# Kernel optimization log

Hardware: AMD Instinct MI355X
Metric: run time of the kernel (lower is better)

The kernel has to match this reference:

```python
import jax, jax.numpy as jnp
import numpy as np

H, W, C = 56, 56, 384
WS, SHIFT, HEADS = 7, 3, 12
HEAD_DIM = C // HEADS
SCALE = HEAD_DIM ** (-0.5)
NWIN = (H // WS) * (W // WS)  # 64 windows per image
NTOK = WS * WS                # 49 tokens per window
EPS = 1e-5


def _gen_mask():
    # static shift-window attention mask, computed with numpy (jit-safe constant)
    img = np.zeros((H, W))
    sl = (slice(0, -WS), slice(-WS, -SHIFT), slice(-SHIFT, None))
    cnt = 0
    for hs in sl:
        for ws in sl:
            img[hs, ws] = cnt
            cnt += 1
    mw = img.reshape(H // WS, WS, W // WS, WS).transpose(0, 2, 1, 3).reshape(-1, NTOK)
    diff = mw[:, None, :] - mw[:, :, None]  # (NWIN, NTOK, NTOK)
    return jnp.asarray(np.where(diff != 0, -100.0, 0.0), dtype=jnp.float32)

ATTN_MASK = _gen_mask()


def _layernorm(x, g, b):
    mu = jnp.mean(x, axis=-1, keepdims=True)
    var = jnp.var(x, axis=-1, keepdims=True)
    return (x - mu) * jax.lax.rsqrt(var + EPS) * g + b


def setup_inputs() -> dict:
    key = jax.random.key(0)
    ks = jax.random.split(key, 6)
    s = 0.02
    return {
        "x": jax.random.normal(ks[0], (16, H * W, C), dtype=jnp.float32),
        "ln1_g": jnp.ones((C,), jnp.float32),
        "ln1_b": jnp.zeros((C,), jnp.float32),
        "qkv_w": jax.random.normal(ks[1], (C, 3 * C), jnp.float32) * s,
        "proj_w": jax.random.normal(ks[2], (C, C), jnp.float32) * s,
        "proj_b": jnp.zeros((C,), jnp.float32),
        "ln2_g": jnp.ones((C,), jnp.float32),
        "ln2_b": jnp.zeros((C,), jnp.float32),
        "fc1_w": jax.random.normal(ks[3], (C, 4 * C), jnp.float32) * s,
        "fc1_b": jnp.zeros((4 * C,), jnp.float32),
        "fc2_w": jax.random.normal(ks[4], (4 * C, C), jnp.float32) * s,
        "fc2_b": jnp.zeros((C,), jnp.float32),
    }


def reference(x, ln1_g, ln1_b, qkv_w, proj_w, proj_b, ln2_g, ln2_b, fc1_w, fc1_b, fc2_w, fc2_b):
    B, N, _ = x.shape
    h = x
    y = _layernorm(x, ln1_g, ln1_b).reshape(B, H, W, C)
    # cyclic shift (note: source never rolls back; we match it)
    y = jnp.roll(y, shift=(-SHIFT, -SHIFT), axis=(1, 2))
    # window partition -> (B*NWIN, NTOK, C)
    y = y.reshape(B, H // WS, WS, W // WS, WS, C).transpose(0, 1, 3, 2, 4, 5)
    y = y.reshape(B * NWIN, NTOK, C)
    # qkv (no bias), split heads
    qkv = (y @ qkv_w).reshape(B * NWIN, NTOK, 3, HEADS, HEAD_DIM)
    qkv = qkv.transpose(2, 0, 3, 1, 4)  # (3, BW, heads, NTOK, hd)
    q, k, v = qkv[0], qkv[1], qkv[2]
    attn = jnp.einsum('whnd,whmd->whnm', q, k) * SCALE  # (BW, heads, NTOK, NTOK)
    attn = attn.reshape(B, NWIN, HEADS, NTOK, NTOK) + ATTN_MASK[None, :, None]
    attn = jax.nn.softmax(attn.reshape(B * NWIN, HEADS, NTOK, NTOK), axis=-1)
    o = jnp.einsum('whnm,whmd->whnd', attn, v)
    o = o.transpose(0, 2, 1, 3).reshape(B * NWIN, NTOK, C)
    o = o @ proj_w + proj_b
    # window reverse -> (B, N, C)
    o = o.reshape(B, H // WS, W // WS, WS, WS, C).transpose(0, 1, 3, 2, 4, 5)
    o = o.reshape(B, N, C)
    x1 = h + o
    # MLP (GELU after both fc1 and fc2, as in source)
    m = _layernorm(x1, ln2_g, ln2_b)
    m = jax.nn.gelu(m @ fc1_w + fc1_b, approximate=False)
    m = jax.nn.gelu(m @ fc2_w + fc2_b, approximate=False)
    return x1 + m
```

## Files before the change

kernel.cpp:

```cpp
#include <hip/hip_runtime.h>
#include <hip/hip_bf16.h>
#include <cstdint>
#include <cstddef>

#define C_DIM   384
#define NIMG    3136
#define MROWS   50176
#define QK_SCALE 0.17677669529663687f

using bf16x8 = __attribute__((ext_vector_type(8))) short;
using f32x4  = __attribute__((ext_vector_type(4))) float;

__device__ __forceinline__ short f2bf(float f) {
  union { float f; uint32_t u; } v; v.f = f;
  uint32_t r = (v.u + 0x7fffu + ((v.u >> 16) & 1u)) >> 16;
  return (short)(uint16_t)r;
}

__device__ __forceinline__ float bf2f(short s) {
  union { uint32_t u; float f; } v; v.u = ((uint32_t)(uint16_t)s) << 16;
  return v.f;
}

__device__ __forceinline__ void async_copy16(const void* g, void* l) {
  __builtin_amdgcn_global_load_lds(
      (const __attribute__((address_space(1))) void*)g,
      (__attribute__((address_space(3))) void*)l, 16, 0, 0);
}

__device__ __forceinline__ float gelu_fast(float x) {
  float x2 = x * x;
  float u = fmaf(0.0356774081f, x2, 0.7978845608f);
  float e = exp2f(x * u * 2.8853900818f);
  float r = __builtin_amdgcn_rcpf(e + 1.0f);
  return fmaf(-x, r, x);
}

__global__ __launch_bounds__(256) void transpose_cast(
    const float* __restrict__ w, short* __restrict__ wt, int K, int N) {
  int idx = blockIdx.x * 256 + threadIdx.x;
  if (idx >= K * N) return;
  int k = idx / N;
  int n = idx - k * N;
  wt[(size_t)n * K + k] = f2bf(w[idx]);
}

template <typename IN>
__global__ __launch_bounds__(256) void ln_kernel(
    const IN* __restrict__ x, const float* __restrict__ g,
    const float* __restrict__ b, short* __restrict__ y, int windowed) {
  int token = blockIdx.x * 4 + (threadIdx.x >> 6);
  int lane = threadIdx.x & 63;
  size_t src;
  if (windowed) {
    int bw = token / 49;
    int tt = token - bw * 49;
    int bb = bw >> 6, w = bw & 63;
    int hs = (w >> 3) * 7 + tt / 7 + 3; if (hs >= 56) hs -= 56;
    int ws = (w & 7) * 7 + (tt % 7) + 3; if (ws >= 56) ws -= 56;
    src = (size_t)(bb * NIMG + hs * 56 + ws) * C_DIM;
  } else {
    src = (size_t)token * C_DIM;
  }
  const IN* xr = x + src;
  float v[6];
  float s = 0.f;
#pragma unroll
  for (int i = 0; i < 6; ++i) {
    if constexpr (sizeof(IN) == 4) v[i] = (float)xr[lane + i * 64];
    else v[i] = bf2f((short)xr[lane + i * 64]);
    s += v[i];
  }
#pragma unroll
  for (int m = 1; m < 64; m <<= 1) s += __shfl_xor(s, m);
  float mu = s * (1.0f / 384.0f);
  float var = 0.f;
#pragma unroll
  for (int i = 0; i < 6; ++i) { float d = v[i] - mu; var += d * d; }
#pragma unroll
  for (int m = 1; m < 64; m <<= 1) var += __shfl_xor(var, m);
  float rstd = rsqrtf(var * (1.0f / 384.0f) + 1e-5f);
  short* yr = y + (size_t)token * C_DIM;
#pragma unroll
  for (int i = 0; i < 6; ++i) {
    int c = lane + i * 64;
    yr[c] = f2bf((v[i] - mu) * rstd * g[c] + b[c]);
  }
}

template <int EPI>
__device__ __forceinline__ void gemm_epilogue(
    f32x4 (&acc)[4][4], void* Out, const float* bias, const void* resid,
    int N, int m0, int n0, int wm, int wn, int lrow, int quad) {
#pragma unroll
  for (int i = 0; i < 4; ++i) {
#pragma unroll
    for (int r = 0; r < 4; ++r) {
      int row = m0 + wm * 64 + i * 16 + quad * 4 + r;
      if (EPI == 1) {
        int bw = row / 49;
        int tt = row - bw * 49;
        int bb = bw >> 6, w = bw & 63;
        int nimg = ((w >> 3) * 7 + tt / 7) * 56 + (w & 7) * 7 + (tt % 7);
        size_t obase = ((size_t)(bb * NIMG + nimg)) * C_DIM;
#pragma unroll
        for (int j = 0; j < 4; ++j) {
          int col = n0 + wn * 64 + j * 16 + lrow;
          size_t oi = obase + col;
          ((short*)Out)[oi] =
              f2bf(acc[i][j][r] + bias[col] + ((const float*)resid)[oi]);
        }
      } else {
#pragma unroll
        for (int j = 0; j < 4; ++j) {
          int col = n0 + wn * 64 + j * 16 + lrow;
          float v = acc[i][j][r];
          if (EPI == 0) {
            ((short*)Out)[(size_t)row * N + col] = f2bf(v);
          } else if (EPI == 2) {
            ((short*)Out)[(size_t)row * N + col] = f2bf(gelu_fast(v + bias[col]));
          } else {
            size_t oi = (size_t)row * C_DIM + col;
            ((float*)Out)[oi] =
                bf2f(((const short*)resid)[oi]) + gelu_fast(v + bias[col]);
          }
        }
      }
    }
  }
}

__device__ __forceinline__ void grid_decode(int nby, int& m0, int& n0) {
  const int wg = (int)blockIdx.x;
  const int swz = (wg & 7) * ((int)gridDim.x >> 3) + (wg >> 3);
  const int mb = swz / nby;
  const int nb = swz - mb * nby;
  m0 = mb * 128;
  n0 = nb * 128;
}

template <int EPI>
__global__ __launch_bounds__(256, 4) void gemm_pipe32_kernel(
    const short* __restrict__ A, const short* __restrict__ Bt,
    void* __restrict__ Out, const float* __restrict__ bias,
    const void* __restrict__ resid, int M, int N, int K, int nby) {
  __shared__ __align__(16) short lds[2][128 * 32 * 2];
  const int t = threadIdx.x;
  const int wave = t >> 6, lane = t & 63;
  const int lrow = lane & 15, quad = lane >> 4;
  const int wm = wave & 1, wn = wave >> 1;
  int m0, n0;
  grid_decode(nby, m0, n0);

  f32x4 acc[4][4] = {};
  const int srow = t >> 2;
  const int spos = t & 3;
  const int nt = K >> 5;

  auto stage = [&](int buf, int k0) {
    short* la = &lds[buf][0];
    short* lb = la + 128 * 32;
#pragma unroll
    for (int i = 0; i < 2; ++i) {
      int row = i * 64 + srow;
      int ca = spos ^ ((row >> 1) & 3);
      async_copy16(A + (size_t)(m0 + row) * K + k0 + ca * 8,
                   la + (i * 64 + wave * 16) * 32);
      async_copy16(Bt + (size_t)(n0 + row) * K + k0 + ca * 8,
                   lb + (i * 64 + wave * 16) * 32);
    }
  };

  auto compute = [&](int buf) {
    short* ldsA = &lds[buf][0];
    short* ldsB = ldsA + 128 * 32;
    bf16x8 af[4], bfr[4];
#pragma unroll
    for (int i = 0; i < 4; ++i) {
      int ra = wm * 64 + i * 16 + lrow;
      af[i] = *(const bf16x8*)(ldsA + ra * 32 + ((quad ^ ((ra >> 1) & 3)) * 8));
      int rb = wn * 64 + i * 16 + lrow;
      bfr[i] = *(const bf16x8*)(ldsB + rb * 32 + ((quad ^ ((rb >> 1) & 3)) * 8));
    }
    __builtin_amdgcn_s_setprio(1);
#pragma unroll
    for (int i = 0; i < 4; ++i)
#pragma unroll
      for (int j = 0; j < 4; ++j)
        acc[i][j] = __builtin_amdgcn_mfma_f32_16x16x32_bf16(af[i], bfr[j],
                                                            acc[i][j], 0, 0, 0);
    __builtin_amdgcn_s_setprio(0);
  };

  stage(0, 0);
  for (int kt = 0; kt < nt; ++kt) {
    __builtin_amdgcn_sched_barrier(0);
    if (kt + 1 < nt) {
      stage((kt + 1) & 1, (kt + 1) * 32);
      asm volatile("s_waitcnt vmcnt(4)" ::: "memory");
    } else {
      asm volatile("s_waitcnt vmcnt(0)" ::: "memory");
    }
    __builtin_amdgcn_s_barrier();
    __builtin_amdgcn_sched_barrier(0);
    compute(kt & 1);
    __builtin_amdgcn_sched_barrier(0);
    __builtin_amdgcn_s_barrier();
  }
  gemm_epilogue<EPI>(acc, Out, bias, resid, N, m0, n0, wm, wn, lrow, quad);
}

template <int EPI>
__global__ __launch_bounds__(256, 2) void gemm_pipe64_kernel(
    const short* __restrict__ A, const short* __restrict__ Bt,
    void* __restrict__ Out, const float* __restrict__ bias,
    const void* __restrict__ resid, int M, int N, int K, int nby) {
  __shared__ __align__(16) short lds[2][128 * 64 * 2];
  const int t = threadIdx.x;
  const int wave = t >> 6, lane = t & 63;
  const int lrow = lane & 15, quad = lane >> 4;
  const int wm = wave & 1, wn = wave >> 1;
  int m0, n0;
  grid_decode(nby, m0, n0);

  f32x4 acc[4][4] = {};
  const int srow = t >> 3;
  const int spos = t & 7;
  const int nt = K >> 6;

  auto stage = [&](int buf, int k0) {
    short* la = &lds[buf][0];
    short* lb = la + 128 * 64;
#pragma unroll
    for (int i = 0; i < 4; ++i) {
      int row = i * 32 + srow;
      int ca = spos ^ (row & 7);
      async_copy16(A + (size_t)(m0 + row) * K + k0 + ca * 8,
                   la + (i * 32 + wave * 8) * 64);
      async_copy16(Bt + (size_t)(n0 + row) * K + k0 + ca * 8,
                   lb + (i * 32 + wave * 8) * 64);
    }
  };

  auto compute = [&](int buf) {
    short* ldsA = &lds[buf][0];
    short* ldsB = ldsA + 128 * 64;
#pragma unroll
    for (int ks = 0; ks < 2; ++ks) {
      const int cb = ks * 4;
      bf16x8 af[4], bfr[4];
#pragma unroll
      for (int i = 0; i < 4; ++i) {
        int ra = wm * 64 + i * 16 + lrow;
        af[i] = *(const bf16x8*)(ldsA + ra * 64 + (((cb + quad) ^ (ra & 7)) * 8));
        int rb = wn * 64 + i * 16 + lrow;
        bfr[i] = *(const bf16x8*)(ldsB + rb * 64 + (((cb + quad) ^ (rb & 7)) * 8));
      }
      __builtin_amdgcn_s_setprio(1);
#pragma unroll
      for (int i = 0; i < 4; ++i)
#pragma unroll
        for (int j = 0; j < 4; ++j)
          acc[i][j] = __builtin_amdgcn_mfma_f32_16x16x32_bf16(af[i], bfr[j],
                                                              acc[i][j], 0, 0, 0);
      __builtin_amdgcn_s_setprio(0);
    }
  };

  stage(0, 0);
  for (int kt = 0; kt < nt; ++kt) {
    __builtin_amdgcn_sched_barrier(0);
    if (kt + 1 < nt) {
      stage((kt + 1) & 1, (kt + 1) * 64);
      asm volatile("s_waitcnt vmcnt(8)" ::: "memory");
    } else {
      asm volatile("s_waitcnt vmcnt(0)" ::: "memory");
    }
    __builtin_amdgcn_s_barrier();
    __builtin_amdgcn_sched_barrier(0);
    compute(kt & 1);
    __builtin_amdgcn_sched_barrier(0);
    __builtin_amdgcn_s_barrier();
  }
  gemm_epilogue<EPI>(acc, Out, bias, resid, N, m0, n0, wm, wn, lrow, quad);
}

__global__ __launch_bounds__(256) void attn_kernel(
    const short* __restrict__ qkv, short* __restrict__ o) {
  __shared__ __align__(16) short plds[4][64 * 40];
  __shared__ __align__(16) short vlds[4][32 * 72];
  const int wavei = threadIdx.x >> 6;
  const int lane = threadIdx.x & 63;
  const int gw = blockIdx.x * 4 + wavei;
  const int bw = gw / 12;
  const int h = gw - bw * 12;
  const int w = bw & 63;
  const int lrow = lane & 15, quad = lane >> 4;
  const short* base = qkv + (size_t)bw * 49 * 1152 + h * 32;

  bf16x8 qf[4], kf[4];
#pragma unroll
  for (int i = 0; i < 4; ++i) {
    int tq = i * 16 + lrow;
    const short* p = base + (size_t)tq * 1152 + quad * 8;
    qf[i] = *(const bf16x8*)p;
    kf[i] = *(const bf16x8*)(p + 384);
  }

  short* vw = vlds[wavei];
  {
    bf16x8 vrow[4] = {};
    if (lane < 49) {
      const short* vp = base + 768 + (size_t)lane * 1152;
#pragma unroll
      for (int c = 0; c < 4; ++c) vrow[c] = *(const bf16x8*)(vp + c * 8);
    }
#pragma unroll
    for (int c = 0; c < 4; ++c)
#pragma unroll
      for (int jj = 0; jj < 8; ++jj)
        vw[(c * 8 + jj) * 72 + lane] = vrow[c][jj];
  }

  f32x4 sa[4][4] = {};
#pragma unroll
  for (int i = 0; i < 4; ++i)
#pragma unroll
    for (int j = 0; j < 4; ++j)
      sa[i][j] = __builtin_amdgcn_mfma_f32_16x16x32_bf16(qf[i], kf[j], sa[i][j], 0, 0, 0);

  int tl = lane < 49 ? lane : 0;
  int rr = tl / 7, cc = tl - rr * 7;
  int hs = (w >> 3) * 7 + rr;
  int ws = (w & 7) * 7 + cc;
  int id = (hs < 49 ? 0 : (hs < 53 ? 3 : 6)) + (ws < 49 ? 0 : (ws < 53 ? 1 : 2));

  int idn[4], idm[4][4];
#pragma unroll
  for (int j = 0; j < 4; ++j) idn[j] = __shfl(id, j * 16 + lrow);
#pragma unroll
  for (int i = 0; i < 4; ++i)
#pragma unroll
    for (int r = 0; r < 4; ++r) idm[i][r] = __shfl(id, i * 16 + quad * 4 + r);

#pragma unroll
  for (int i = 0; i < 4; ++i)
#pragma unroll
    for (int j = 0; j < 4; ++j)
#pragma unroll
      for (int r = 0; r < 4; ++r) {
        float v = sa[i][j][r] * QK_SCALE + (idm[i][r] == idn[j] ? 0.f : -100.f);
        sa[i][j][r] = (j * 16 + lrow < 49) ? v : -1e30f;
      }

#pragma unroll
  for (int i = 0; i < 4; ++i)
#pragma unroll
    for (int r = 0; r < 4; ++r) {
      float mx = -1e30f;
#pragma unroll
      for (int j = 0; j < 4; ++j) mx = fmaxf(mx, sa[i][j][r]);
#pragma unroll
      for (int m = 1; m < 16; m <<= 1) mx = fmaxf(mx, __shfl_xor(mx, m));
      float sum = 0.f;
#pragma unroll
      for (int j = 0; j < 4; ++j) {
        float e = exp2f((sa[i][j][r] - mx) * 1.44269504f);
        sa[i][j][r] = e;
        sum += e;
      }
#pragma unroll
      for (int m = 1; m < 16; m <<= 1) sum += __shfl_xor(sum, m);
      float inv = 1.0f / sum;
#pragma unroll
      for (int j = 0; j < 4; ++j) sa[i][j][r] *= inv;
    }

  short* pw = plds[wavei];
  f32x4 oa[4][2] = {};
#pragma unroll
  for (int kk = 0; kk < 2; ++kk) {
#pragma unroll
    for (int jh = 0; jh < 2; ++jh) {
      int j = kk * 2 + jh;
#pragma unroll
      for (int i = 0; i < 4; ++i)
#pragma unroll
        for (int r = 0; r < 4; ++r)
          pw[(i * 16 + quad * 4 + r) * 40 + jh * 16 + lrow] = f2bf(sa[i][j][r]);
    }
    asm volatile("s_waitcnt lgkmcnt(0)" ::: "memory");
    __builtin_amdgcn_sched_barrier(0);

    bf16x8 vf[2];
#pragma unroll
    for (int j2 = 0; j2 < 2; ++j2)
      vf[j2] = *(const bf16x8*)(vw + (j2 * 16 + lrow) * 72 + kk * 32 + quad * 8);
#pragma unroll
    for (int i = 0; i < 4; ++i) {
      bf16x8 pf = *(const bf16x8*)(pw + (i * 16 + lrow) * 40 + quad * 8);
#pragma unroll
      for (int j2 = 0; j2 < 2; ++j2)
        oa[i][j2] = __builtin_amdgcn_mfma_f32_16x16x32_bf16(pf, vf[j2], oa[i][j2], 0, 0, 0);
    }
    asm volatile("s_waitcnt lgkmcnt(0)" ::: "memory");
    __builtin_amdgcn_sched_barrier(0);
  }

#pragma unroll
  for (int i = 0; i < 4; ++i)
#pragma unroll
    for (int j2 = 0; j2 < 2; ++j2)
#pragma unroll
      for (int r = 0; r < 4; ++r) {
        int m = i * 16 + quad * 4 + r;
        if (m < 49)
          o[((size_t)bw * 49 + m) * 384 + h * 32 + j2 * 16 + lrow] = f2bf(oa[i][j2][r]);
      }
}

extern "C" void kernel_launch(void* const* d_in, const int* in_sizes, int n_in,
                              void* d_out, int out_size, void* d_ws, size_t ws_size,
                              hipStream_t stream) {
  const float* x      = (const float*)d_in[0];
  const float* ln1_g  = (const float*)d_in[1];
  const float* ln1_b  = (const float*)d_in[2];
  const float* qkv_w  = (const float*)d_in[3];
  const float* proj_w = (const float*)d_in[4];
  const float* proj_b = (const float*)d_in[5];
  const float* ln2_g  = (const float*)d_in[6];
  const float* ln2_b  = (const float*)d_in[7];
  const float* fc1_w  = (const float*)d_in[8];
  const float* fc1_b  = (const float*)d_in[9];
  const float* fc2_w  = (const float*)d_in[10];
  const float* fc2_b  = (const float*)d_in[11];
  float* out = (float*)d_out;

  char* ws = (char*)d_ws;
  auto alloc = [&](size_t bytes) {
    char* p = ws;
    ws += (bytes + 255) & ~(size_t)255;
    return p;
  };
  short* qkv_wT  = (short*)alloc((size_t)1152 * 384 * 2);
  short* proj_wT = (short*)alloc((size_t)384 * 384 * 2);
  short* fc1_wT  = (short*)alloc((size_t)1536 * 384 * 2);
  short* fc2_wT  = (short*)alloc((size_t)384 * 1536 * 2);
  short* bufA    = (short*)alloc((size_t)MROWS * 384 * 2);
  short* x1      = (short*)alloc((size_t)MROWS * 384 * 2);
  short* bufB    = (short*)alloc((size_t)MROWS * 1536 * 2);

  transpose_cast<<<(384 * 1152) / 256, 256, 0, stream>>>(qkv_w, qkv_wT, 384, 1152);
  transpose_cast<<<(384 * 384) / 256, 256, 0, stream>>>(proj_w, proj_wT, 384, 384);
  transpose_cast<<<(384 * 1536) / 256, 256, 0, stream>>>(fc1_w, fc1_wT, 384, 1536);
  transpose_cast<<<(1536 * 384) / 256, 256, 0, stream>>>(fc2_w, fc2_wT, 1536, 384);

  ln_kernel<float><<<MROWS / 4, 256, 0, stream>>>(x, ln1_g, ln1_b, bufA, 1);

  gemm_pipe32_kernel<0><<<392 * 9, 256, 0, stream>>>(bufA, qkv_wT, bufB, nullptr,
                                                     nullptr, MROWS, 1152, 384, 9);

  attn_kernel<<<3072, 256, 0, stream>>>(bufB, bufA);

  gemm_pipe32_kernel<1><<<392 * 3, 256, 0, stream>>>(bufA, proj_wT, x1, proj_b,
                                                     x, MROWS, 384, 384, 3);

  ln_kernel<short><<<MROWS / 4, 256, 0, stream>>>(x1, ln2_g, ln2_b, bufA, 0);

  gemm_pipe32_kernel<2><<<392 * 12, 256, 0, stream>>>(bufA, fc1_wT, bufB, fc1_b,
                                                      nullptr, MROWS, 1536, 384, 12);

  gemm_pipe64_kernel<3><<<392 * 3, 256, 0, stream>>>(bufB, fc2_wT, out, fc2_b,
                                                     x1, MROWS, 384, 1536, 3);
}
```

Baseline: 521.6 us.

## Load GEMM B operand directly from global into registers, bypassing LDS

```diff
diff --git a/kernel.cpp b/kernel.cpp
--- a/kernel.cpp
+++ b/kernel.cpp
@@ -144,7 +144,7 @@
     const short* __restrict__ A, const short* __restrict__ Bt,
     void* __restrict__ Out, const float* __restrict__ bias,
     const void* __restrict__ resid, int M, int N, int K, int nby) {
-  __shared__ __align__(16) short lds[2][128 * 32 * 2];
+  __shared__ __align__(16) short lds[2][128 * 32];
   const int t = threadIdx.x;
   const int wave = t >> 6, lane = t & 63;
   const int lrow = lane & 15, quad = lane >> 4;
@@ -157,30 +157,32 @@
   const int spos = t & 3;
   const int nt = K >> 5;
 
-  auto stage = [&](int buf, int k0) {
+  auto stageA = [&](int buf, int k0) {
     short* la = &lds[buf][0];
-    short* lb = la + 128 * 32;
 #pragma unroll
     for (int i = 0; i < 2; ++i) {
       int row = i * 64 + srow;
       int ca = spos ^ ((row >> 1) & 3);
       async_copy16(A + (size_t)(m0 + row) * K + k0 + ca * 8,
                    la + (i * 64 + wave * 16) * 32);
-      async_copy16(Bt + (size_t)(n0 + row) * K + k0 + ca * 8,
-                   lb + (i * 64 + wave * 16) * 32);
-    }
-  };
-
-  auto compute = [&](int buf) {
+    }
+  };
+
+  auto loadB = [&](bf16x8 (&b)[4], int k0) {
+#pragma unroll
+    for (int j = 0; j < 4; ++j) {
+      int rb = n0 + wn * 64 + j * 16 + lrow;
+      b[j] = *(const bf16x8*)(Bt + (size_t)rb * K + k0 + quad * 8);
+    }
+  };
+
+  auto compute = [&](int buf, bf16x8 (&bfr)[4]) {
     short* ldsA = &lds[buf][0];
-    short* ldsB = ldsA + 128 * 32;
-    bf16x8 af[4], bfr[4];
+    bf16x8 af[4];
 #pragma unroll
     for (int i = 0; i < 4; ++i) {
       int ra = wm * 64 + i * 16 + lrow;
       af[i] = *(const bf16x8*)(ldsA + ra * 32 + ((quad ^ ((ra >> 1) & 3)) * 8));
-      int rb = wn * 64 + i * 16 + lrow;
-      bfr[i] = *(const bf16x8*)(ldsB + rb * 32 + ((quad ^ ((rb >> 1) & 3)) * 8));
     }
     __builtin_amdgcn_s_setprio(1);
 #pragma unroll
@@ -192,18 +194,30 @@
     __builtin_amdgcn_s_setprio(0);
   };
 
-  stage(0, 0);
-  for (int kt = 0; kt < nt; ++kt) {
-    __builtin_amdgcn_sched_barrier(0);
-    if (kt + 1 < nt) {
-      stage((kt + 1) & 1, (kt + 1) * 32);
-      asm volatile("s_waitcnt vmcnt(4)" ::: "memory");
+  bf16x8 b0[4], b1[4];
+  stageA(0, 0);
+  loadB(b0, 0);
+  for (int kt = 0; kt < nt; kt += 2) {
+    __builtin_amdgcn_sched_barrier(0);
+    stageA(1, (kt + 1) * 32);
+    loadB(b1, (kt + 1) * 32);
+    asm volatile("s_waitcnt vmcnt(6)" ::: "memory");
+    __builtin_amdgcn_s_barrier();
+    __builtin_amdgcn_sched_barrier(0);
+    compute(0, b0);
+    __builtin_amdgcn_sched_barrier(0);
+    __builtin_amdgcn_s_barrier();
+    __builtin_amdgcn_sched_barrier(0);
+    if (kt + 2 < nt) {
+      stageA(0, (kt + 2) * 32);
+      loadB(b0, (kt + 2) * 32);
+      asm volatile("s_waitcnt vmcnt(6)" ::: "memory");
     } else {
       asm volatile("s_waitcnt vmcnt(0)" ::: "memory");
     }
     __builtin_amdgcn_s_barrier();
     __builtin_amdgcn_sched_barrier(0);
-    compute(kt & 1);
+    compute(1, b1);
     __builtin_amdgcn_sched_barrier(0);
     __builtin_amdgcn_s_barrier();
   }
@@ -215,7 +229,7 @@
     const short* __restrict__ A, const short* __restrict__ Bt,
     void* __restrict__ Out, const float* __restrict__ bias,
     const void* __restrict__ resid, int M, int N, int K, int nby) {
-  __shared__ __align__(16) short lds[2][128 * 64 * 2];
+  __shared__ __align__(16) short lds[2][128 * 64];
   const int t = threadIdx.x;
   const int wave = t >> 6, lane = t & 63;
   const int lrow = lane & 15, quad = lane >> 4;
@@ -228,57 +242,74 @@
   const int spos = t & 7;
   const int nt = K >> 6;
 
-  auto stage = [&](int buf, int k0) {
+  auto stageA = [&](int buf, int k0) {
     short* la = &lds[buf][0];
-    short* lb = la + 128 * 64;
 #pragma unroll
     for (int i = 0; i < 4; ++i) {
       int row = i * 32 + srow;
       int ca = spos ^ (row & 7);
       async_copy16(A + (size_t)(m0 + row) * K + k0 + ca * 8,
                    la + (i * 32 + wave * 8) * 64);
-      async_copy16(Bt + (size_t)(n0 + row) * K + k0 + ca * 8,
-                   lb + (i * 32 + wave * 8) * 64);
-    }
-  };
-
-  auto compute = [&](int buf) {
+    }
+  };
+
+  auto loadB = [&](bf16x8 (&b)[2][4], int k0) {
+#pragma unroll
+    for (int ks = 0; ks < 2; ++ks)
+#pragma unroll
+      for (int j = 0; j < 4; ++j) {
+        int rb = n0 + wn * 64 + j * 16 + lrow;
+        b[ks][j] = *(const bf16x8*)(Bt + (size_t)rb * K + k0 + (ks * 4 + quad) * 8);
+      }
+  };
+
+  auto compute = [&](int buf, bf16x8 (&b)[2][4]) {
     short* ldsA = &lds[buf][0];
-    short* ldsB = ldsA + 128 * 64;
 #pragma unroll
     for (int ks = 0; ks < 2; ++ks) {
       const int cb = ks * 4;
-      bf16x8 af[4], bfr[4];
+      bf16x8 af[4];
 #pragma unroll
       for (int i = 0; i < 4; ++i) {
         int ra = wm * 64 + i * 16 + lrow;
         af[i] = *(const bf16x8*)(ldsA + ra * 64 + (((cb + quad) ^ (ra & 7)) * 8));
-        int rb = wn * 64 + i * 16 + lrow;
-        bfr[i] = *(const bf16x8*)(ldsB + rb * 64 + (((cb + quad) ^ (rb & 7)) * 8));
       }
       __builtin_amdgcn_s_setprio(1);
 #pragma unroll
       for (int i = 0; i < 4; ++i)
 #pragma unroll
         for (int j = 0; j < 4; ++j)
-          acc[i][j] = __builtin_amdgcn_mfma_f32_16x16x32_bf16(af[i], bfr[j],
+          acc[i][j] = __builtin_amdgcn_mfma_f32_16x16x32_bf16(af[i], b[ks][j],
                                                               acc[i][j], 0, 0, 0);
       __builtin_amdgcn_s_setprio(0);
     }
   };
 
-  stage(0, 0);
-  for (int kt = 0; kt < nt; ++kt) {
-    __builtin_amdgcn_sched_barrier(0);
-    if (kt + 1 < nt) {
-      stage((kt + 1) & 1, (kt + 1) * 64);
-      asm volatile("s_waitcnt vmcnt(8)" ::: "memory");
+  bf16x8 b0[2][4], b1[2][4];
+  stageA(0, 0);
+  loadB(b0, 0);
+  for (int kt = 0; kt < nt; kt += 2) {
+    __builtin_amdgcn_sched_barrier(0);
+    stageA(1, (kt + 1) * 64);
+    loadB(b1, (kt + 1) * 64);
+    asm volatile("s_waitcnt vmcnt(12)" ::: "memory");
+    __builtin_amdgcn_s_barrier();
+    __builtin_amdgcn_sched_barrier(0);
+    compute(0, b0);
+    __builtin_amdgcn_sched_barrier(0);
+    __builtin_amdgcn_s_barrier();
+
+    __builtin_amdgcn_sched_barrier(0);
+    if (kt + 2 < nt) {
+      stageA(0, (kt + 2) * 64);
+      loadB(b0, (kt + 2) * 64);
+      asm volatile("s_waitcnt vmcnt(12)" ::: "memory");
     } else {
       asm volatile("s_waitcnt vmcnt(0)" ::: "memory");
     }
     __builtin_amdgcn_s_barrier();
     __builtin_amdgcn_sched_barrier(0);
-    compute(kt & 1);
+    compute(1, b1);
     __builtin_amdgcn_sched_barrier(0);
     __builtin_amdgcn_s_barrier();
   }
```

New measurement: 878.7 us. +68.4%, slower.

## Load B tiles directly to registers in pipe32 GEMM, halve LDS

Applied to the files above, without the earlier changes.

```diff
diff --git a/kernel.cpp b/kernel.cpp
--- a/kernel.cpp
+++ b/kernel.cpp
@@ -140,11 +140,11 @@
 }
 
 template <int EPI>
-__global__ __launch_bounds__(256, 4) void gemm_pipe32_kernel(
+__global__ __launch_bounds__(256, 3) void gemm_pipe32_kernel(
     const short* __restrict__ A, const short* __restrict__ Bt,
     void* __restrict__ Out, const float* __restrict__ bias,
     const void* __restrict__ resid, int M, int N, int K, int nby) {
-  __shared__ __align__(16) short lds[2][128 * 32 * 2];
+  __shared__ __align__(16) short lds[2][128 * 32];
   const int t = threadIdx.x;
   const int wave = t >> 6, lane = t & 63;
   const int lrow = lane & 15, quad = lane >> 4;
@@ -157,30 +157,32 @@
   const int spos = t & 3;
   const int nt = K >> 5;
 
-  auto stage = [&](int buf, int k0) {
+  auto stageA = [&](int buf, int k0) {
     short* la = &lds[buf][0];
-    short* lb = la + 128 * 32;
 #pragma unroll
     for (int i = 0; i < 2; ++i) {
       int row = i * 64 + srow;
       int ca = spos ^ ((row >> 1) & 3);
       async_copy16(A + (size_t)(m0 + row) * K + k0 + ca * 8,
                    la + (i * 64 + wave * 16) * 32);
-      async_copy16(Bt + (size_t)(n0 + row) * K + k0 + ca * 8,
-                   lb + (i * 64 + wave * 16) * 32);
-    }
-  };
-
-  auto compute = [&](int buf) {
+    }
+  };
+
+  auto loadB = [&](bf16x8 (&b)[4], int k0) {
+#pragma unroll
+    for (int j = 0; j < 4; ++j) {
+      int rb = n0 + wn * 64 + j * 16 + lrow;
+      b[j] = *(const bf16x8*)(Bt + (size_t)rb * K + k0 + quad * 8);
+    }
+  };
+
+  auto compute = [&](int buf, bf16x8 (&bfr)[4]) {
     short* ldsA = &lds[buf][0];
-    short* ldsB = ldsA + 128 * 32;
-    bf16x8 af[4], bfr[4];
+    bf16x8 af[4];
 #pragma unroll
     for (int i = 0; i < 4; ++i) {
       int ra = wm * 64 + i * 16 + lrow;
       af[i] = *(const bf16x8*)(ldsA + ra * 32 + ((quad ^ ((ra >> 1) & 3)) * 8));
-      int rb = wn * 64 + i * 16 + lrow;
-      bfr[i] = *(const bf16x8*)(ldsB + rb * 32 + ((quad ^ ((rb >> 1) & 3)) * 8));
     }
     __builtin_amdgcn_s_setprio(1);
 #pragma unroll
@@ -192,18 +194,30 @@
     __builtin_amdgcn_s_setprio(0);
   };
 
-  stage(0, 0);
-  for (int kt = 0; kt < nt; ++kt) {
-    __builtin_amdgcn_sched_barrier(0);
-    if (kt + 1 < nt) {
-      stage((kt + 1) & 1, (kt + 1) * 32);
-      asm volatile("s_waitcnt vmcnt(4)" ::: "memory");
+  bf16x8 b0[4], b1[4];
+  stageA(0, 0);
+  loadB(b0, 0);
+  for (int kt = 0; kt < nt; kt += 2) {
+    __builtin_amdgcn_sched_barrier(0);
+    stageA(1, (kt + 1) * 32);
+    loadB(b1, (kt + 1) * 32);
+    asm volatile("s_waitcnt vmcnt(6)" ::: "memory");
+    __builtin_amdgcn_s_barrier();
+    __builtin_amdgcn_sched_barrier(0);
+    compute(0, b0);
+    __builtin_amdgcn_sched_barrier(0);
+    __builtin_amdgcn_s_barrier();
+    __builtin_amdgcn_sched_barrier(0);
+    if (kt + 2 < nt) {
+      stageA(0, (kt + 2) * 32);
+      loadB(b0, (kt + 2) * 32);
+      asm volatile("s_waitcnt vmcnt(6)" ::: "memory");
     } else {
       asm volatile("s_waitcnt vmcnt(0)" ::: "memory");
     }
     __builtin_amdgcn_s_barrier();
     __builtin_amdgcn_sched_barrier(0);
-    compute(kt & 1);
+    compute(1, b1);
     __builtin_amdgcn_sched_barrier(0);
     __builtin_amdgcn_s_barrier();
   }
```

Result: slower. 616.6 us (+18.2%).
